# Optimization experiments

Measured on AMD Instinct MI355X. Metric: run time of the kernel, lower is better.

The kernel has to match this reference:

```python
import jax, jax.numpy as jnp
import numpy as np

D_IN, D_OUT, K = 128, 256, 16
B, N = 2, 16384
D_HALF = D_OUT // 2
EPS = 1e-6
GROUPS = 16


def conv1x1(x, w, b):
    # x: (B,C,N,K), w: (O,C), b: (O,)
    return jnp.einsum('oc,bcnk->bonk', w, x) + b[None, :, None, None]


def groupnorm(x, w, b, groups=GROUPS):
    Bv, C, Nv, Kv = x.shape
    xr = x.reshape(Bv, groups, C // groups, Nv, Kv)
    m = xr.mean(axis=(2, 3, 4), keepdims=True)
    v = xr.var(axis=(2, 3, 4), keepdims=True)
    xn = ((xr - m) / jnp.sqrt(v + EPS)).reshape(Bv, C, Nv, Kv)
    return xn * w[None, :, None, None] + b[None, :, None, None]


def lse(coords, x, idx, dist, w, b, gw, gb):
    # coords: (B,N,3); x: (B,C,N,1); idx: (B,N,K); dist: (B,N,K)
    nbr = jax.vmap(lambda c, i: c[i])(coords, idx)          # (B,N,K,3)
    ctr = jnp.broadcast_to(coords[:, :, None, :], nbr.shape)  # (B,N,K,3)
    rel = jnp.concatenate([ctr, nbr, ctr - nbr], axis=-1)    # (B,N,K,9)
    geo = jnp.concatenate([rel.transpose(0, 3, 1, 2), dist[:, None, :, :]], axis=1)  # (B,10,N,K)
    geo = jax.nn.relu(groupnorm(conv1x1(geo, w, b), gw, gb))  # (B,d/2,N,K)
    nf = jax.vmap(lambda f, i: f[:, i])(x[..., 0], idx)       # (B,d/2,N,K)
    return jnp.concatenate([geo, nf], axis=1)                 # (B,d,N,K)


def attentive_pool(x, w, b, gw, gb):
    m = x.mean(axis=-1, keepdims=True)  # (B,C,N,1)
    return jax.nn.relu(groupnorm(conv1x1(m, w, b), gw, gb))


def setup_inputs() -> dict:
    key = jax.random.key(0)
    ks = jax.random.split(key, 16)
    s = 0.02
    d = {
        'coords': jax.random.normal(ks[0], (B, N, 3), jnp.float32),
        'features': jax.random.normal(ks[1], (B, D_IN, N, 1), jnp.float32),
        'knn_dist': jax.random.uniform(ks[2], (B, N, K), jnp.float32),
        'knn_idx': jax.random.randint(ks[3], (B, N, K), 0, N),
        'w1': jax.random.normal(ks[4], (D_HALF, D_IN), jnp.float32) * s,
        'b1': jnp.zeros((D_HALF,), jnp.float32),
        'lse1_w': jax.random.normal(ks[5], (D_HALF, 10), jnp.float32) * s,
        'lse1_b': jnp.zeros((D_HALF,), jnp.float32),
        'lse1_gw': jnp.ones((D_HALF,), jnp.float32),
        'lse1_gb': jnp.zeros((D_HALF,), jnp.float32),
        'pool1_w': jax.random.normal(ks[6], (D_HALF, D_OUT), jnp.float32) * s,
        'pool1_b': jnp.zeros((D_HALF,), jnp.float32),
        'pool1_gw': jnp.ones((D_HALF,), jnp.float32),
        'pool1_gb': jnp.zeros((D_HALF,), jnp.float32),
        'lse2_w': jax.random.normal(ks[7], (D_HALF, 10), jnp.float32) * s,
        'lse2_b': jnp.zeros((D_HALF,), jnp.float32),
        'lse2_gw': jnp.ones((D_HALF,), jnp.float32),
        'lse2_gb': jnp.zeros((D_HALF,), jnp.float32),
        'pool2_w': jax.random.normal(ks[8], (D_OUT, D_OUT), jnp.float32) * s,
        'pool2_b': jnp.zeros((D_OUT,), jnp.float32),
        'pool2_gw': jnp.ones((D_OUT,), jnp.float32),
        'pool2_gb': jnp.zeros((D_OUT,), jnp.float32),
        'mlp2_w': jax.random.normal(ks[9], (2 * D_OUT, D_OUT), jnp.float32) * s,
        'mlp2_b': jnp.zeros((2 * D_OUT,), jnp.float32),
        'sc_w': jax.random.normal(ks[10], (2 * D_OUT, D_IN), jnp.float32) * s,
        'sc_b': jnp.zeros((2 * D_OUT,), jnp.float32),
        'sc_gw': jnp.ones((2 * D_OUT,), jnp.float32),
        'sc_gb': jnp.zeros((2 * D_OUT,), jnp.float32),
    }
    return d


def reference(coords, features, knn_dist, knn_idx,
              w1, b1,
              lse1_w, lse1_b, lse1_gw, lse1_gb,
              pool1_w, pool1_b, pool1_gw, pool1_gb,
              lse2_w, lse2_b, lse2_gw, lse2_gb,
              pool2_w, pool2_b, pool2_gw, pool2_gb,
              mlp2_w, mlp2_b, sc_w, sc_b, sc_gw, sc_gb):
    # mlp1: conv + LeakyReLU(0.2), no norm
    x = jax.nn.leaky_relu(conv1x1(features, w1, b1), 0.2)        # (B,d/2,N,1)
    x = lse(coords, x, knn_idx, knn_dist, lse1_w, lse1_b, lse1_gw, lse1_gb)  # (B,d,N,K)
    x = attentive_pool(x, pool1_w, pool1_b, pool1_gw, pool1_gb)  # (B,d/2,N,1)
    x = lse(coords, x, knn_idx, knn_dist, lse2_w, lse2_b, lse2_gw, lse2_gb)  # (B,d,N,K)
    x = attentive_pool(x, pool2_w, pool2_b, pool2_gw, pool2_gb)  # (B,d,N,1)
    main = conv1x1(x, mlp2_w, mlp2_b)                            # (B,2d,N,1)
    short = groupnorm(conv1x1(features, sc_w, sc_b), sc_gw, sc_gb)
    return jax.nn.leaky_relu(main + short, 0.01)                 # (B,2d,N,1)
```

## Files before the change

kernel.cpp:

```cpp
#include <hip/hip_runtime.h>


constexpr int Bc = 2;
constexpr int Nc = 16384;
constexpr int Kc = 16;
constexpr float EPSc = 1e-6f;

typedef __attribute__((ext_vector_type(8))) short short8;
typedef __attribute__((ext_vector_type(4))) short short4v;
typedef __attribute__((ext_vector_type(4))) float floatx4;

__device__ inline short f2bf(float x) {
    union { float f; unsigned u; } v; v.f = x;
    unsigned r = v.u + 0x7fffu + ((v.u >> 16) & 1u);
    return (short)(r >> 16);
}
__device__ inline float bf2f(short s) {
    union { unsigned u; float f; } v;
    v.u = ((unsigned)(unsigned short)s) << 16;
    return v.f;
}

constexpr size_t OW_P1W = 0;
constexpr size_t OW_P2W = OW_P1W + 128*256;
constexpr size_t OW_M2W = OW_P2W + 256*256;
constexpr size_t OW_SCW = OW_M2W + 512*256;
constexpr size_t OW_W1  = OW_SCW + 512*128;
constexpr size_t OW_L1W = OW_W1  + 128*128;
constexpr size_t OW_L2W = OW_L1W + 128*32;
constexpr size_t OW_FB  = OW_L2W + 128*32;
constexpr size_t OW_X1  = OW_FB  + (size_t)Bc*Nc*128;
constexpr size_t OW_M   = OW_X1  + (size_t)Bc*Nc*128;
constexpr size_t OW_Z1  = OW_M   + (size_t)Bc*Nc*256;
constexpr size_t OW_Z2  = OW_Z1  + (size_t)Bc*Nc*128;
constexpr size_t OW_S   = OW_Z2  + (size_t)Bc*Nc*256;

constexpr int CV0 = 128*256;
constexpr int CV1 = CV0 + 256*256;
constexpr int CV2 = CV1 + 512*256;
constexpr int CV3 = CV2 + 512*128;
constexpr int CV4 = CV3 + 128*128;
constexpr int CV5 = CV4 + 128*32;
constexpr int CV6 = CV5 + 128*32;
constexpr int CVTOT = CV6 + 512;

__global__ void prep_kernel(const float* __restrict__ p1w,
                            const float* __restrict__ p2w,
                            const float* __restrict__ m2w,
                            const float* __restrict__ scw,
                            const float* __restrict__ w1,
                            const float* __restrict__ l1w,
                            const float* __restrict__ l2w,
                            short* __restrict__ W16,
                            float* __restrict__ ST)
{
    int i = blockIdx.x * 256 + threadIdx.x;
    if (i < CV0) { W16[OW_P1W + i] = f2bf(p1w[i]); return; }
    if (i < CV1) { int k = i - CV0; W16[OW_P2W + k] = f2bf(p2w[k]); return; }
    if (i < CV2) { int k = i - CV1; W16[OW_M2W + k] = f2bf(m2w[k]); return; }
    if (i < CV3) { int k = i - CV2; W16[OW_SCW + k] = f2bf(scw[k]); return; }
    if (i < CV4) { int k = i - CV3; W16[OW_W1  + k] = f2bf(w1[k]); return; }
    if (i < CV5) { int k = i - CV4; int o = k >> 5, c = k & 31;
                   W16[OW_L1W + k] = (c < 10) ? f2bf(l1w[o*10+c]) : (short)0; return; }
    if (i < CV6) { int k = i - CV5; int o = k >> 5, c = k & 31;
                   W16[OW_L2W + k] = (c < 10) ? f2bf(l2w[o*10+c]) : (short)0; return; }
    { int k = i - CV6; if (k < 512) ST[k] = 0.f; }
}

__global__ void feat_t_kernel(const float* __restrict__ in, short* __restrict__ out) {
    int tid  = threadIdx.x;
    int lane = tid & 63, wave = tid >> 6;
    int bb = blockIdx.x / (Nc / 64);
    int n  = (blockIdx.x % (Nc / 64)) * 64 + lane;
    #pragma unroll
    for (int cc = 0; cc < 4; cc++) {
        int c0 = (wave + cc * 4) * 8;
        short8 sv;
        #pragma unroll
        for (int i = 0; i < 8; i++)
            sv[i] = f2bf(in[((size_t)bb * 128 + c0 + i) * Nc + n]);
        *(short8*)&out[((size_t)(bb * Nc + n)) * 128 + c0] = sv;
    }
}

__launch_bounds__(256)
__global__ void geo_reduce_kernel(const float* __restrict__ coords,
                                  const int* __restrict__ knn_idx,
                                  const float* __restrict__ knn_dist,
                                  float* __restrict__ dst)
{
    __shared__ float part[4][65];
    const int tid  = threadIdx.x;
    const int b    = blockIdx.y;
    const int base = blockIdx.x * 256 + tid;
    const float* cb  = coords   + (size_t)b * Nc * 3;
    const int*   ib  = knn_idx  + (size_t)b * Nc * Kc;
    const float* db  = knn_dist + (size_t)b * Nc * Kc;

    float acc[65];
    #pragma unroll
    for (int i = 0; i < 65; i++) acc[i] = 0.f;

    #pragma unroll
    for (int it = 0; it < 4; it++) {
        int r = base + it * 65536;
        int n = r >> 4;
        float cx = cb[n*3+0], cy = cb[n*3+1], cz = cb[n*3+2];
        int   j  = ib[r];
        float nx = cb[j*3+0], ny = cb[j*3+1], nz = cb[j*3+2];
        float d  = db[r];
        float g[10] = {cx,cy,cz,nx,ny,nz,cx-nx,cy-ny,cz-nz,d};
        #pragma unroll
        for (int c = 0; c < 10; c++) acc[c] += g[c];
        int idx = 10;
        #pragma unroll
        for (int c = 0; c < 10; c++)
            #pragma unroll
            for (int c2 = c; c2 < 10; c2++) acc[idx++] += g[c] * g[c2];
    }
    #pragma unroll
    for (int i = 0; i < 65; i++) {
        float v = acc[i];
        #pragma unroll
        for (int off = 1; off < 64; off <<= 1) v += __shfl_xor(v, off);
        acc[i] = v;
    }
    int lane = tid & 63, wave = tid >> 6;
    if (lane == 0) {
        #pragma unroll
        for (int i = 0; i < 65; i++) part[wave][i] = acc[i];
    }
    __syncthreads();
    if (tid < 65) {
        float s = part[0][tid] + part[1][tid] + part[2][tid] + part[3][tid];
        atomicAdd(&dst[b * 65 + tid], s);
    }
}

__launch_bounds__(512)
__global__ void lse_param_kernel(const float* __restrict__ geoS,
                                 const float* __restrict__ l1w,
                                 const float* __restrict__ l1b,
                                 const float* __restrict__ l1gw,
                                 const float* __restrict__ l1gb,
                                 const float* __restrict__ l2w,
                                 const float* __restrict__ l2b,
                                 const float* __restrict__ l2gw,
                                 const float* __restrict__ l2gb,
                                 float* __restrict__ lp)
{
    __shared__ float osum[512], osq[512];
    const int tid = threadIdx.x;
    const int s = tid >> 8, r = tid & 255, b = r >> 7, o = r & 127;
    const float* wf = s ? l2w : l1w;
    const float* bf = s ? l2b : l1b;
    const float* gwf = s ? l2gw : l1gw;
    const float* gbf = s ? l2gb : l1gb;
    const float NK = (float)(Nc * Kc);
    const float* S = geoS + b * 65;

    float w[10];
    #pragma unroll
    for (int c = 0; c < 10; c++) w[c] = wf[o * 10 + c];
    float wS = 0.f;
    #pragma unroll
    for (int c = 0; c < 10; c++) wS += w[c] * S[c];
    float q = 0.f;
    {
        int idx = 10;
        #pragma unroll
        for (int c = 0; c < 10; c++)
            #pragma unroll
            for (int c2 = c; c2 < 10; c2++) {
                float t = w[c] * w[c2] * S[idx++];
                q += (c == c2) ? t : 2.f * t;
            }
    }
    float bo = bf[o];
    osum[tid] = NK * bo + wS;
    osq[tid]  = NK * bo * bo + 2.f * bo * wS + q;
    __syncthreads();
    int gb0 = tid & ~7;
    float gs = 0.f, gq = 0.f;
    #pragma unroll
    for (int i = 0; i < 8; i++) { gs += osum[gb0 + i]; gq += osq[gb0 + i]; }
    float cnt  = 8.f * NK;
    float mean = gs / cnt;
    float var  = gq / cnt - mean * mean;
    float iv   = rsqrtf(var + EPSc);
    float psc  = iv * gwf[o];
    float psh  = (bo - mean) * psc + gbf[o];
    lp[s * 512 + b * 256 + o]       = psc;
    lp[s * 512 + b * 256 + 128 + o] = psh;
}

template<int CIN, int COUT, int GROUP_CH, int MODE>
__launch_bounds__(256)
__global__ void gemm_conv(const short* __restrict__ wA,
                          const short* __restrict__ xB,
                          const float* __restrict__ bias,
                          short* __restrict__ outb,
                          float* __restrict__ outf,
                          float* __restrict__ stats,
                          const short* __restrict__ sbuf,
                          const float* __restrict__ st_sc,
                          const float* __restrict__ gw,
                          const float* __restrict__ gb,
                          float sc_cnt,
                          const float* __restrict__ bst,
                          const float* __restrict__ bgw,
                          const float* __restrict__ bgb,
                          float bcnt,
                          const float* __restrict__ bias2,
                          short* __restrict__ outb2)
{
    __shared__ short Abuf[128 * 68];
    __shared__ short Bbuf[128 * 68];
    __shared__ float sstat[32];
    __shared__ float smean[4], sinv[4];
    __shared__ float bsc[256], bsh[256];

    const int tid  = threadIdx.x;
    const int n0   = blockIdx.x * 128;
    const int mo   = blockIdx.y * 128;
    const int b    = blockIdx.z;
    const int lane = tid & 63;
    const int wave = tid >> 6;
    const int wm   = (wave >> 1) * 64;
    const int wn   = (wave & 1) * 64;
    const int l15  = lane & 15;
    const int quad = lane >> 4;
    const bool sc_tile = (MODE == 4) && (mo < 512);

    if constexpr (MODE == 2 || MODE == 4) { if (tid < 32) sstat[tid] = 0.f; }
    if constexpr (MODE == 3) {
        if (tid < 4) {
            int g = (mo >> 5) + tid;
            float s0 = st_sc[(b * 16 + g) * 2 + 0];
            float s1 = st_sc[(b * 16 + g) * 2 + 1];
            float mean = s0 / sc_cnt;
            float var  = s1 / sc_cnt - mean * mean;
            smean[tid] = mean;
            sinv[tid]  = rsqrtf(var + EPSc);
        }
        if (tid < CIN) {
            int g = tid >> 4;
            float s0 = bst[(b * 16 + g) * 2 + 0];
            float s1 = bst[(b * 16 + g) * 2 + 1];
            float mean = s0 / bcnt;
            float var  = s1 / bcnt - mean * mean;
            float inv  = rsqrtf(var + EPSc);
            float sc_  = inv * bgw[tid];
            bsc[tid] = sc_;
            bsh[tid] = bgb[tid] - mean * sc_;
        }
    }

    floatx4 acc[4][4];
    #pragma unroll
    for (int mi = 0; mi < 4; mi++)
        #pragma unroll
        for (int ni = 0; ni < 4; ni++)
            acc[mi][ni] = (floatx4){0.f, 0.f, 0.f, 0.f};

    const short* wAr = wA + (size_t)mo * CIN;
    const short* xBr = xB + (size_t)b * Nc * CIN + (size_t)n0 * CIN;

    for (int c0 = 0; c0 < CIN; c0 += 64) {
        __syncthreads();
        #pragma unroll
        for (int s = 0; s < 4; s++) {
            int e = tid + s * 256;
            int r = e >> 3, q = e & 7;
            *(short8*)&Abuf[r * 68 + q * 8] =
                *(const short8*)(wAr + (size_t)r * CIN + c0 + q * 8);
            short8 v = *(const short8*)(xBr + (size_t)r * CIN + c0 + q * 8);
            if constexpr (MODE == 3) {
                #pragma unroll
                for (int i = 0; i < 8; i++) {
                    int ch = c0 + q * 8 + i;
                    float t = bf2f(v[i]) * bsc[ch] + bsh[ch];
                    v[i] = f2bf(t > 0.f ? t : 0.f);
                }
            }
            *(short8*)&Bbuf[r * 68 + q * 8] = v;
        }
        __syncthreads();

        #pragma unroll
        for (int kk = 0; kk < 2; kk++) {
            short8 af[4], bfr[4];
            #pragma unroll
            for (int mi = 0; mi < 4; mi++)
                af[mi] = *(short8*)&Abuf[(wm + mi * 16 + l15) * 68 + kk * 32 + quad * 8];
            #pragma unroll
            for (int ni = 0; ni < 4; ni++)
                bfr[ni] = *(short8*)&Bbuf[(wn + ni * 16 + l15) * 68 + kk * 32 + quad * 8];
            #pragma unroll
            for (int mi = 0; mi < 4; mi++)
                #pragma unroll
                for (int ni = 0; ni < 4; ni++)
                    acc[mi][ni] = __builtin_amdgcn_mfma_f32_16x16x32_bf16(
                        af[mi], bfr[ni], acc[mi][ni], 0, 0, 0);
        }
    }

    #pragma unroll
    for (int mi = 0; mi < 4; mi++) {
        int rowl = wm + mi * 16 + quad * 4;
        float b4[4], gw4[4], gb4[4];
        #pragma unroll
        for (int r = 0; r < 4; r++) {
            if constexpr (MODE == 4) {
                b4[r] = sc_tile ? bias[mo + rowl + r] : bias2[mo - 512 + rowl + r];
            } else {
                b4[r] = bias[mo + rowl + r];
            }
            if constexpr (MODE == 3) {
                gw4[r] = gw[mo + rowl + r];
                gb4[r] = gb[mo + rowl + r];
            }
        }
        float gs = 0.f, gq = 0.f;
        #pragma unroll
        for (int ni = 0; ni < 4; ni++) {
            int col = n0 + wn + ni * 16 + l15;
            if constexpr (MODE == 3) {
                short4v s4 = *(const short4v*)&sbuf[((size_t)(b * Nc + col)) * 512 + mo + rowl];
                int gl = rowl >> 5;
                #pragma unroll
                for (int r = 0; r < 4; r++) {
                    float v = acc[mi][ni][r] + b4[r];
                    float s = bf2f(s4[r]);
                    float sn = (s - smean[gl]) * sinv[gl] * gw4[r] + gb4[r];
                    float o = v + sn;
                    o = o > 0.f ? o : 0.01f * o;
                    outf[((size_t)b * COUT + mo + rowl + r) * Nc + col] = o;
                }
            } else if constexpr (MODE == 4) {
                short4v sv;
                #pragma unroll
                for (int r = 0; r < 4; r++) {
                    float v = acc[mi][ni][r] + b4[r];
                    if (sc_tile) { gs += v; gq += v * v; }
                    else v = v > 0.f ? v : 0.2f * v;
                    sv[r] = f2bf(v);
                }
                if (sc_tile)
                    *(short4v*)&outb[((size_t)(b * Nc + col)) * 512 + mo + rowl] = sv;
                else
                    *(short4v*)&outb2[((size_t)(b * Nc + col)) * 128 + mo - 512 + rowl] = sv;
            } else {
                short4v sv;
                #pragma unroll
                for (int r = 0; r < 4; r++) {
                    float v = acc[mi][ni][r] + b4[r];
                    if constexpr (MODE == 1) v = v > 0.f ? v : 0.2f * v;
                    if constexpr (MODE == 2) { gs += v; gq += v * v; }
                    sv[r] = f2bf(v);
                }
                *(short4v*)&outb[((size_t)(b * Nc + col)) * COUT + mo + rowl] = sv;
            }
        }
        if ((MODE == 2) || (MODE == 4 && sc_tile)) {
            #pragma unroll
            for (int off = 1; off < 16; off <<= 1) {
                gs += __shfl_xor(gs, off);
                gq += __shfl_xor(gq, off);
            }
            if (l15 == 0) {
                int gl = rowl / GROUP_CH;
                atomicAdd(&sstat[gl * 2 + 0], gs);
                atomicAdd(&sstat[gl * 2 + 1], gq);
            }
        }
    }
    if ((MODE == 2) || (MODE == 4 && sc_tile)) {
        __syncthreads();
        constexpr int NG = 128 / GROUP_CH;
        if (tid < 2 * NG) {
            int g0 = mo / GROUP_CH;
            atomicAdd(&stats[b * 32 + (g0 + (tid >> 1)) * 2 + (tid & 1)], sstat[tid]);
        }
    }
}

__launch_bounds__(256)
__global__ void lse_m_kernel(const float* __restrict__ coords,
                             const int* __restrict__ knn_idx,
                             const float* __restrict__ knn_dist,
                             const short* __restrict__ xprev,
                             const short* __restrict__ wpad,
                             const float* __restrict__ lp,
                             const float* __restrict__ xst,
                             const float* __restrict__ xgw,
                             const float* __restrict__ xgb,
                             float xcnt,
                             short* __restrict__ m)
{
    __shared__ short Bbuf[256 * 40];
    __shared__ int   jl[256];
    __shared__ float xscs[128], xshs[128];

    const int tid = threadIdx.x;
    const int b   = blockIdx.x >> 10;
    const int n0  = (blockIdx.x & 1023) * 16;
    const bool norm = (xst != nullptr);

    const int lane = tid & 63, wave = tid >> 6;
    const int l15 = lane & 15, quad = lane >> 4;

    short8 af0 = *(const short8*)(wpad + ((wave * 2 + 0) * 16 + l15) * 32 + quad * 8);
    short8 af1 = *(const short8*)(wpad + ((wave * 2 + 1) * 16 + l15) * 32 + quad * 8);
    floatx4 psc0 = *(const floatx4*)&lp[b * 256 + (wave * 2 + 0) * 16 + quad * 4];
    floatx4 psh0 = *(const floatx4*)&lp[b * 256 + 128 + (wave * 2 + 0) * 16 + quad * 4];
    floatx4 psc1 = *(const floatx4*)&lp[b * 256 + (wave * 2 + 1) * 16 + quad * 4];
    floatx4 psh1 = *(const floatx4*)&lp[b * 256 + 128 + (wave * 2 + 1) * 16 + quad * 4];

    if (norm && tid < 128) {
        int g = tid >> 3;
        float s0 = xst[(b * 16 + g) * 2 + 0];
        float s1 = xst[(b * 16 + g) * 2 + 1];
        float mean = s0 / xcnt;
        float var  = s1 / xcnt - mean * mean;
        float inv  = rsqrtf(var + EPSc);
        float sc_  = inv * xgw[tid];
        xscs[tid] = sc_;
        xshs[tid] = xgb[tid] - mean * sc_;
    }
    {
        int pt = tid & 15, k = tid >> 4;
        int n  = n0 + pt;
        const float* cb = coords + (size_t)b * Nc * 3;
        float cx = cb[n*3+0], cy = cb[n*3+1], cz = cb[n*3+2];
        int   j  = knn_idx[((size_t)b * Nc + n) * Kc + k];
        float nx = cb[j*3+0], ny = cb[j*3+1], nz = cb[j*3+2];
        float d  = knn_dist[((size_t)b * Nc + n) * Kc + k];
        int col = k * 16 + pt;
        short8 w0, w1, zz;
        w0[0]=f2bf(cx); w0[1]=f2bf(cy); w0[2]=f2bf(cz);
        w0[3]=f2bf(nx); w0[4]=f2bf(ny); w0[5]=f2bf(nz);
        w0[6]=f2bf(cx-nx); w0[7]=f2bf(cy-ny);
        w1[0]=f2bf(cz-nz); w1[1]=f2bf(d);
        #pragma unroll
        for (int i = 2; i < 8; i++) w1[i] = 0;
        #pragma unroll
        for (int i = 0; i < 8; i++) zz[i] = 0;
        *(short8*)&Bbuf[col * 40 + 0]  = w0;
        *(short8*)&Bbuf[col * 40 + 8]  = w1;
        *(short8*)&Bbuf[col * 40 + 16] = zz;
        *(short8*)&Bbuf[col * 40 + 24] = zz;
        jl[col] = j;
    }
    __syncthreads();

    #pragma unroll
    for (int mt2 = 0; mt2 < 2; mt2++) {
        const int mt = wave * 2 + mt2;
        const short8 af = mt2 ? af1 : af0;
        const floatx4 psc4 = mt2 ? psc1 : psc0;
        const floatx4 psh4 = mt2 ? psh1 : psh0;
        float s4[4] = {0.f, 0.f, 0.f, 0.f};
        #pragma unroll
        for (int nb = 0; nb < 8; nb++) {
            short8 f0 = *(short8*)&Bbuf[((nb * 2 + 0) * 16 + l15) * 40 + quad * 8];
            short8 f1 = *(short8*)&Bbuf[((nb * 2 + 1) * 16 + l15) * 40 + quad * 8];
            floatx4 a0 = __builtin_amdgcn_mfma_f32_16x16x32_bf16(
                af, f0, (floatx4){0.f, 0.f, 0.f, 0.f}, 0, 0, 0);
            floatx4 a1 = __builtin_amdgcn_mfma_f32_16x16x32_bf16(
                af, f1, (floatx4){0.f, 0.f, 0.f, 0.f}, 0, 0, 0);
            #pragma unroll
            for (int r = 0; r < 4; r++) {
                float v0 = a0[r] * psc4[r] + psh4[r];
                float v1 = a1[r] * psc4[r] + psh4[r];
                s4[r] += (v0 > 0.f ? v0 : 0.f) + (v1 > 0.f ? v1 : 0.f);
            }
        }
        short4v sv;
        #pragma unroll
        for (int r = 0; r < 4; r++) sv[r] = f2bf(s4[r] * (1.f / 16.f));
        *(short4v*)&m[((size_t)(b * Nc + n0 + l15)) * 256 + mt * 16 + quad * 4] = sv;
    }

    {
        const int tp = tid >> 4, cs = tid & 15;
        float sc8[8], sh8[8];
        if (norm) {
            #pragma unroll
            for (int i = 0; i < 8; i++) { sc8[i] = xscs[cs*8+i]; sh8[i] = xshs[cs*8+i]; }
        }
        float acc8[8];
        #pragma unroll
        for (int i = 0; i < 8; i++) acc8[i] = 0.f;
        #pragma unroll
        for (int k = 0; k < 16; k++) {
            int j = jl[k * 16 + tp];
            short8 v = *(const short8*)&xprev[((size_t)(b * Nc + j)) * 128 + cs * 8];
            if (norm) {
                #pragma unroll
                for (int i = 0; i < 8; i++) {
                    float t = bf2f(v[i]) * sc8[i] + sh8[i];
                    acc8[i] += t > 0.f ? t : 0.f;
                }
            } else {
                #pragma unroll
                for (int i = 0; i < 8; i++) acc8[i] += bf2f(v[i]);
            }
        }
        short8 sv;
        #pragma unroll
        for (int i = 0; i < 8; i++) sv[i] = f2bf(acc8[i] * (1.f / 16.f));
        *(short8*)&m[((size_t)(b * Nc + n0 + tp)) * 256 + 128 + cs * 8] = sv;
    }
}

extern "C" void kernel_launch(void* const* d_in, const int* in_sizes, int n_in,
                              void* d_out, int out_size, void* d_ws, size_t ws_size,
                              hipStream_t stream)
{
    const float* coords   = (const float*)d_in[0];
    const float* features = (const float*)d_in[1];
    const float* knn_dist = (const float*)d_in[2];
    const int*   knn_idx  = (const int*)  d_in[3];
    const float* w1       = (const float*)d_in[4];
    const float* b1       = (const float*)d_in[5];
    const float* lse1_w   = (const float*)d_in[6];
    const float* lse1_b   = (const float*)d_in[7];
    const float* lse1_gw  = (const float*)d_in[8];
    const float* lse1_gb  = (const float*)d_in[9];
    const float* pool1_w  = (const float*)d_in[10];
    const float* pool1_b  = (const float*)d_in[11];
    const float* pool1_gw = (const float*)d_in[12];
    const float* pool1_gb = (const float*)d_in[13];
    const float* lse2_w   = (const float*)d_in[14];
    const float* lse2_b   = (const float*)d_in[15];
    const float* lse2_gw  = (const float*)d_in[16];
    const float* lse2_gb  = (const float*)d_in[17];
    const float* pool2_w  = (const float*)d_in[18];
    const float* pool2_b  = (const float*)d_in[19];
    const float* pool2_gw = (const float*)d_in[20];
    const float* pool2_gb = (const float*)d_in[21];
    const float* mlp2_w   = (const float*)d_in[22];
    const float* mlp2_b   = (const float*)d_in[23];
    const float* sc_w     = (const float*)d_in[24];
    const float* sc_b     = (const float*)d_in[25];
    const float* sc_gw    = (const float*)d_in[26];
    const float* sc_gb    = (const float*)d_in[27];
    (void)in_sizes; (void)n_in; (void)out_size; (void)ws_size;

    float* ST = (float*)d_ws;
    float* ST_SC  = ST + 0;
    float* ST_P1  = ST + 64;
    float* ST_P2  = ST + 128;
    float* ST_GEO = ST + 256;
    float* ST_LP  = ST + 512;
    short* W16 = (short*)(ST + 2048);
    short* P1Wb = W16 + OW_P1W;
    short* P2Wb = W16 + OW_P2W;
    short* M2Wb = W16 + OW_M2W;
    short* SCWb = W16 + OW_SCW;
    short* L1Wb = W16 + OW_L1W;
    short* L2Wb = W16 + OW_L2W;
    short* FB   = W16 + OW_FB;
    short* X1B  = W16 + OW_X1;
    short* MB   = W16 + OW_M;
    short* Z1   = W16 + OW_Z1;
    short* Z2   = W16 + OW_Z2;
    short* SB   = W16 + OW_S;
    float* out  = (float*)d_out;

    prep_kernel<<<(CVTOT + 255) / 256, 256, 0, stream>>>(
        pool1_w, pool2_w, mlp2_w, sc_w, w1, lse1_w, lse2_w, W16, ST);
    feat_t_kernel<<<Bc * Nc / 64, 256, 0, stream>>>(features, FB);
    geo_reduce_kernel<<<dim3(256, Bc), 256, 0, stream>>>(
        coords, knn_idx, knn_dist, ST_GEO);
    lse_param_kernel<<<1, 512, 0, stream>>>(
        ST_GEO, lse1_w, lse1_b, lse1_gw, lse1_gb,
        lse2_w, lse2_b, lse2_gw, lse2_gb, ST_LP);

    gemm_conv<128,640,32,4><<<dim3(Nc/128, 5, Bc), 256, 0, stream>>>(
        SCWb, FB, sc_b, SB, nullptr, ST_SC, nullptr, nullptr, nullptr, nullptr, 0.f,
        nullptr, nullptr, nullptr, 0.f, b1, X1B);
    lse_m_kernel<<<Bc * Nc / 16, 256, 0, stream>>>(
        coords, knn_idx, knn_dist, X1B, L1Wb, ST_LP,
        nullptr, nullptr, nullptr, 0.f, MB);
    gemm_conv<256,128,8,2><<<dim3(Nc/128, 1, Bc), 256, 0, stream>>>(
        P1Wb, MB, pool1_b, Z1, nullptr, ST_P1, nullptr, nullptr, nullptr, nullptr, 0.f,
        nullptr, nullptr, nullptr, 0.f, nullptr, nullptr);
    lse_m_kernel<<<Bc * Nc / 16, 256, 0, stream>>>(
        coords, knn_idx, knn_dist, Z1, L2Wb, ST_LP + 512,
        ST_P1, pool1_gw, pool1_gb, (float)(8 * Nc), MB);
    gemm_conv<256,256,16,2><<<dim3(Nc/128, 2, Bc), 256, 0, stream>>>(
        P2Wb, MB, pool2_b, Z2, nullptr, ST_P2, nullptr, nullptr, nullptr, nullptr, 0.f,
        nullptr, nullptr, nullptr, 0.f, nullptr, nullptr);
    gemm_conv<256,512,32,3><<<dim3(Nc/128, 4, Bc), 256, 0, stream>>>(
        M2Wb, Z2, mlp2_b, nullptr, out, nullptr, SB, ST_SC, sc_gw, sc_gb,
        (float)(32 * Nc), ST_P2, pool2_gw, pool2_gb, (float)(16 * Nc),
        nullptr, nullptr);
}
```

Baseline: 305.6 us.

## Fuse LSE neighbor-mean kernel with attentive-pool GEMM via shared-memory tile

Merges the LSE kernel, which builds the pooled 256-channel vector per point, with the following pool 1x1-conv GEMM. Each 512-thread block now handles 64 points and keeps the pooled tile in swizzled LDS. It then runs the pool conv with MFMA, writes Z, and accumulates the groupnorm statistics. This removes the global write and re-read of the intermediate M buffer and two kernel launches. In exchange it uses more LDS per block, which may lower occupancy, and adds block-level syncs between the four geometry passes.

```diff
diff --git a/kernel.cpp b/kernel.cpp
--- a/kernel.cpp
+++ b/kernel.cpp
@@ -385,38 +385,37 @@
     }
 }
 
-__launch_bounds__(256)
-__global__ void lse_m_kernel(const float* __restrict__ coords,
-                             const int* __restrict__ knn_idx,
-                             const float* __restrict__ knn_dist,
-                             const short* __restrict__ xprev,
-                             const short* __restrict__ wpad,
-                             const float* __restrict__ lp,
-                             const float* __restrict__ xst,
-                             const float* __restrict__ xgw,
-                             const float* __restrict__ xgb,
-                             float xcnt,
-                             short* __restrict__ m)
+template<int PCOUT, int PGROUP>
+__launch_bounds__(512)
+__global__ void lse_pool_kernel(const float* __restrict__ coords,
+                                const int* __restrict__ knn_idx,
+                                const float* __restrict__ knn_dist,
+                                const short* __restrict__ xprev,
+                                const short* __restrict__ wpad,
+                                const float* __restrict__ lp,
+                                const float* __restrict__ xst,
+                                const float* __restrict__ xgw,
+                                const float* __restrict__ xgb,
+                                float xcnt,
+                                const short* __restrict__ pw,
+                                const float* __restrict__ pb,
+                                float* __restrict__ stats,
+                                short* __restrict__ z)
 {
     __shared__ short Bbuf[256 * 40];
-    __shared__ int   jl[256];
+    __shared__ short mld[64 * 256];
+    __shared__ int   jl[1024];
     __shared__ float xscs[128], xshs[128];
+    __shared__ float sstat[32];
 
     const int tid = threadIdx.x;
-    const int b   = blockIdx.x >> 10;
-    const int n0  = (blockIdx.x & 1023) * 16;
+    const int b   = blockIdx.x >> 8;
+    const int n0  = (blockIdx.x & 255) * 64;
     const bool norm = (xst != nullptr);
-
     const int lane = tid & 63, wave = tid >> 6;
     const int l15 = lane & 15, quad = lane >> 4;
 
-    short8 af0 = *(const short8*)(wpad + ((wave * 2 + 0) * 16 + l15) * 32 + quad * 8);
-    short8 af1 = *(const short8*)(wpad + ((wave * 2 + 1) * 16 + l15) * 32 + quad * 8);
-    floatx4 psc0 = *(const floatx4*)&lp[b * 256 + (wave * 2 + 0) * 16 + quad * 4];
-    floatx4 psh0 = *(const floatx4*)&lp[b * 256 + 128 + (wave * 2 + 0) * 16 + quad * 4];
-    floatx4 psc1 = *(const floatx4*)&lp[b * 256 + (wave * 2 + 1) * 16 + quad * 4];
-    floatx4 psh1 = *(const floatx4*)&lp[b * 256 + 128 + (wave * 2 + 1) * 16 + quad * 4];
-
+    if (tid < 32) sstat[tid] = 0.f;
     if (norm && tid < 128) {
         int g = tid >> 3;
         float s0 = xst[(b * 16 + g) * 2 + 0];
@@ -428,58 +427,65 @@
         xscs[tid] = sc_;
         xshs[tid] = xgb[tid] - mean * sc_;
     }
-    {
-        int pt = tid & 15, k = tid >> 4;
-        int n  = n0 + pt;
-        const float* cb = coords + (size_t)b * Nc * 3;
-        float cx = cb[n*3+0], cy = cb[n*3+1], cz = cb[n*3+2];
-        int   j  = knn_idx[((size_t)b * Nc + n) * Kc + k];
-        float nx = cb[j*3+0], ny = cb[j*3+1], nz = cb[j*3+2];
-        float d  = knn_dist[((size_t)b * Nc + n) * Kc + k];
-        int col = k * 16 + pt;
-        short8 w0, w1, zz;
-        w0[0]=f2bf(cx); w0[1]=f2bf(cy); w0[2]=f2bf(cz);
-        w0[3]=f2bf(nx); w0[4]=f2bf(ny); w0[5]=f2bf(nz);
-        w0[6]=f2bf(cx-nx); w0[7]=f2bf(cy-ny);
-        w1[0]=f2bf(cz-nz); w1[1]=f2bf(d);
-        #pragma unroll
-        for (int i = 2; i < 8; i++) w1[i] = 0;
-        #pragma unroll
-        for (int i = 0; i < 8; i++) zz[i] = 0;
-        *(short8*)&Bbuf[col * 40 + 0]  = w0;
-        *(short8*)&Bbuf[col * 40 + 8]  = w1;
-        *(short8*)&Bbuf[col * 40 + 16] = zz;
-        *(short8*)&Bbuf[col * 40 + 24] = zz;
-        jl[col] = j;
-    }
-    __syncthreads();
-
-    #pragma unroll
-    for (int mt2 = 0; mt2 < 2; mt2++) {
-        const int mt = wave * 2 + mt2;
-        const short8 af = mt2 ? af1 : af0;
-        const floatx4 psc4 = mt2 ? psc1 : psc0;
-        const floatx4 psh4 = mt2 ? psh1 : psh0;
-        float s4[4] = {0.f, 0.f, 0.f, 0.f};
-        #pragma unroll
-        for (int nb = 0; nb < 8; nb++) {
-            short8 f0 = *(short8*)&Bbuf[((nb * 2 + 0) * 16 + l15) * 40 + quad * 8];
-            short8 f1 = *(short8*)&Bbuf[((nb * 2 + 1) * 16 + l15) * 40 + quad * 8];
-            floatx4 a0 = __builtin_amdgcn_mfma_f32_16x16x32_bf16(
-                af, f0, (floatx4){0.f, 0.f, 0.f, 0.f}, 0, 0, 0);
-            floatx4 a1 = __builtin_amdgcn_mfma_f32_16x16x32_bf16(
-                af, f1, (floatx4){0.f, 0.f, 0.f, 0.f}, 0, 0, 0);
-            #pragma unroll
-            for (int r = 0; r < 4; r++) {
-                float v0 = a0[r] * psc4[r] + psh4[r];
-                float v1 = a1[r] * psc4[r] + psh4[r];
-                s4[r] += (v0 > 0.f ? v0 : 0.f) + (v1 > 0.f ? v1 : 0.f);
-            }
-        }
-        short4v sv;
-        #pragma unroll
-        for (int r = 0; r < 4; r++) sv[r] = f2bf(s4[r] * (1.f / 16.f));
-        *(short4v*)&m[((size_t)(b * Nc + n0 + l15)) * 256 + mt * 16 + quad * 4] = sv;
+
+    short8 af = *(const short8*)(wpad + (wave * 16 + l15) * 32 + quad * 8);
+    floatx4 psc = *(const floatx4*)&lp[b * 256 + wave * 16 + quad * 4];
+    floatx4 psh = *(const floatx4*)&lp[b * 256 + 128 + wave * 16 + quad * 4];
+
+    const float* cb = coords + (size_t)b * Nc * 3;
+
+    #pragma unroll
+    for (int pass = 0; pass < 4; pass++) {
+        if (tid < 256) {
+            int ptl = tid & 15, k = tid >> 4;
+            int p = pass * 16 + ptl;
+            int n = n0 + p;
+            float cx = cb[n*3+0], cy = cb[n*3+1], cz = cb[n*3+2];
+            int   j  = knn_idx[((size_t)b * Nc + n) * Kc + k];
+            float nx = cb[j*3+0], ny = cb[j*3+1], nz = cb[j*3+2];
+            float d  = knn_dist[((size_t)b * Nc + n) * Kc + k];
+            int col = k * 16 + ptl;
+            short8 w0, w1, zz;
+            w0[0]=f2bf(cx); w0[1]=f2bf(cy); w0[2]=f2bf(cz);
+            w0[3]=f2bf(nx); w0[4]=f2bf(ny); w0[5]=f2bf(nz);
+            w0[6]=f2bf(cx-nx); w0[7]=f2bf(cy-ny);
+            w1[0]=f2bf(cz-nz); w1[1]=f2bf(d);
+            #pragma unroll
+            for (int i = 2; i < 8; i++) w1[i] = 0;
+            #pragma unroll
+            for (int i = 0; i < 8; i++) zz[i] = 0;
+            *(short8*)&Bbuf[col * 40 + 0]  = w0;
+            *(short8*)&Bbuf[col * 40 + 8]  = w1;
+            *(short8*)&Bbuf[col * 40 + 16] = zz;
+            *(short8*)&Bbuf[col * 40 + 24] = zz;
+            jl[k * 64 + p] = j;
+        }
+        __syncthreads();
+        {
+            float s4[4] = {0.f, 0.f, 0.f, 0.f};
+            #pragma unroll
+            for (int nb = 0; nb < 8; nb++) {
+                short8 f0 = *(short8*)&Bbuf[((nb*2+0)*16 + l15) * 40 + quad * 8];
+                short8 f1 = *(short8*)&Bbuf[((nb*2+1)*16 + l15) * 40 + quad * 8];
+                floatx4 a0 = __builtin_amdgcn_mfma_f32_16x16x32_bf16(
+                    af, f0, (floatx4){0.f, 0.f, 0.f, 0.f}, 0, 0, 0);
+                floatx4 a1 = __builtin_amdgcn_mfma_f32_16x16x32_bf16(
+                    af, f1, (floatx4){0.f, 0.f, 0.f, 0.f}, 0, 0, 0);
+                #pragma unroll
+                for (int r = 0; r < 4; r++) {
+                    float v0 = a0[r] * psc[r] + psh[r];
+                    float v1 = a1[r] * psc[r] + psh[r];
+                    s4[r] += (v0 > 0.f ? v0 : 0.f) + (v1 > 0.f ? v1 : 0.f);
+                }
+            }
+            int p = pass * 16 + l15;
+            int g = wave * 2 + (quad >> 1);
+            short4v sv;
+            #pragma unroll
+            for (int r = 0; r < 4; r++) sv[r] = f2bf(s4[r] * (1.f / 16.f));
+            *(short4v*)&mld[p * 256 + ((g ^ (p & 7)) << 3) + (quad & 1) * 4] = sv;
+        }
+        __syncthreads();
     }
 
     {
@@ -489,29 +495,85 @@
             #pragma unroll
             for (int i = 0; i < 8; i++) { sc8[i] = xscs[cs*8+i]; sh8[i] = xshs[cs*8+i]; }
         }
-        float acc8[8];
-        #pragma unroll
-        for (int i = 0; i < 8; i++) acc8[i] = 0.f;
-        #pragma unroll
-        for (int k = 0; k < 16; k++) {
-            int j = jl[k * 16 + tp];
-            short8 v = *(const short8*)&xprev[((size_t)(b * Nc + j)) * 128 + cs * 8];
-            if (norm) {
-                #pragma unroll
-                for (int i = 0; i < 8; i++) {
-                    float t = bf2f(v[i]) * sc8[i] + sh8[i];
-                    acc8[i] += t > 0.f ? t : 0.f;
+        #pragma unroll
+        for (int pp = 0; pp < 2; pp++) {
+            int p = tp + pp * 32;
+            float acc8[8];
+            #pragma unroll
+            for (int i = 0; i < 8; i++) acc8[i] = 0.f;
+            #pragma unroll
+            for (int k = 0; k < 16; k++) {
+                int j = jl[k * 64 + p];
+                short8 v = *(const short8*)&xprev[((size_t)(b * Nc + j)) * 128 + cs * 8];
+                if (norm) {
+                    #pragma unroll
+                    for (int i = 0; i < 8; i++) {
+                        float t = bf2f(v[i]) * sc8[i] + sh8[i];
+                        acc8[i] += t > 0.f ? t : 0.f;
+                    }
+                } else {
+                    #pragma unroll
+                    for (int i = 0; i < 8; i++) acc8[i] += bf2f(v[i]);
                 }
-            } else {
-                #pragma unroll
-                for (int i = 0; i < 8; i++) acc8[i] += bf2f(v[i]);
-            }
-        }
-        short8 sv;
-        #pragma unroll
-        for (int i = 0; i < 8; i++) sv[i] = f2bf(acc8[i] * (1.f / 16.f));
-        *(short8*)&m[((size_t)(b * Nc + n0 + tp)) * 256 + 128 + cs * 8] = sv;
-    }
+            }
+            short8 sv;
+            #pragma unroll
+            for (int i = 0; i < 8; i++) sv[i] = f2bf(acc8[i] * (1.f / 16.f));
+            int g = 16 + cs;
+            *(short8*)&mld[p * 256 + ((g ^ (p & 7)) << 3)] = sv;
+        }
+    }
+    __syncthreads();
+
+    constexpr int NOT = PCOUT / 128;
+    #pragma unroll
+    for (int oi = 0; oi < NOT; oi++) {
+        const int ot = wave + oi * 8;
+        short8 afk[8];
+        #pragma unroll
+        for (int ks = 0; ks < 8; ks++)
+            afk[ks] = *(const short8*)(pw + ((size_t)(ot * 16 + l15)) * 256 + ks * 32 + quad * 8);
+        floatx4 acc[4];
+        #pragma unroll
+        for (int nt = 0; nt < 4; nt++) acc[nt] = (floatx4){0.f, 0.f, 0.f, 0.f};
+        #pragma unroll
+        for (int ks = 0; ks < 8; ks++) {
+            #pragma unroll
+            for (int nt = 0; nt < 4; nt++) {
+                int p = nt * 16 + l15;
+                int g = ks * 4 + quad;
+                short8 bfr = *(short8*)&mld[p * 256 + ((g ^ (p & 7)) << 3)];
+                acc[nt] = __builtin_amdgcn_mfma_f32_16x16x32_bf16(
+                    afk[ks], bfr, acc[nt], 0, 0, 0);
+            }
+        }
+        floatx4 b4 = *(const floatx4*)&pb[ot * 16 + quad * 4];
+        float gs = 0.f, gq = 0.f;
+        #pragma unroll
+        for (int nt = 0; nt < 4; nt++) {
+            int col = n0 + nt * 16 + l15;
+            short4v sv;
+            #pragma unroll
+            for (int r = 0; r < 4; r++) {
+                float v = acc[nt][r] + b4[r];
+                gs += v; gq += v * v;
+                sv[r] = f2bf(v);
+            }
+            *(short4v*)&z[((size_t)(b * Nc + col)) * PCOUT + ot * 16 + quad * 4] = sv;
+        }
+        #pragma unroll
+        for (int off = 1; off < 16; off <<= 1) {
+            gs += __shfl_xor(gs, off);
+            gq += __shfl_xor(gq, off);
+        }
+        if (l15 == 0) {
+            int gl = (ot * 16 + quad * 4) / PGROUP;
+            atomicAdd(&sstat[gl * 2 + 0], gs);
+            atomicAdd(&sstat[gl * 2 + 1], gq);
+        }
+    }
+    __syncthreads();
+    if (tid < 32) atomicAdd(&stats[b * 32 + tid], sstat[tid]);
 }
 
 extern "C" void kernel_launch(void* const* d_in, const int* in_sizes, int n_in,
@@ -563,7 +625,6 @@
     short* L2Wb = W16 + OW_L2W;
     short* FB   = W16 + OW_FB;
     short* X1B  = W16 + OW_X1;
-    short* MB   = W16 + OW_M;
     short* Z1   = W16 + OW_Z1;
     short* Z2   = W16 + OW_Z2;
     short* SB   = W16 + OW_S;
@@ -581,18 +642,14 @@
     gemm_conv<128,640,32,4><<<dim3(Nc/128, 5, Bc), 256, 0, stream>>>(
         SCWb, FB, sc_b, SB, nullptr, ST_SC, nullptr, nullptr, nullptr, nullptr, 0.f,
         nullptr, nullptr, nullptr, 0.f, b1, X1B);
-    lse_m_kernel<<<Bc * Nc / 16, 256, 0, stream>>>(
+    lse_pool_kernel<128,8><<<Bc * Nc / 64, 512, 0, stream>>>(
         coords, knn_idx, knn_dist, X1B, L1Wb, ST_LP,
-        nullptr, nullptr, nullptr, 0.f, MB);
-    gemm_conv<256,128,8,2><<<dim3(Nc/128, 1, Bc), 256, 0, stream>>>(
-        P1Wb, MB, pool1_b, Z1, nullptr, ST_P1, nullptr, nullptr, nullptr, nullptr, 0.f,
-        nullptr, nullptr, nullptr, 0.f, nullptr, nullptr);
-    lse_m_kernel<<<Bc * Nc / 16, 256, 0, stream>>>(
+        nullptr, nullptr, nullptr, 0.f,
+        P1Wb, pool1_b, ST_P1, Z1);
+    lse_pool_kernel<256,16><<<Bc * Nc / 64, 512, 0, stream>>>(
         coords, knn_idx, knn_dist, Z1, L2Wb, ST_LP + 512,
-        ST_P1, pool1_gw, pool1_gb, (float)(8 * Nc), MB);
-    gemm_conv<256,256,16,2><<<dim3(Nc/128, 2, Bc), 256, 0, stream>>>(
-        P2Wb, MB, pool2_b, Z2, nullptr, ST_P2, nullptr, nullptr, nullptr, nullptr, 0.f,
-        nullptr, nullptr, nullptr, 0.f, nullptr, nullptr);
+        ST_P1, pool1_gw, pool1_gb, (float)(8 * Nc),
+        P2Wb, pool2_b, ST_P2, Z2);
     gemm_conv<256,512,32,3><<<dim3(Nc/128, 4, Bc), 256, 0, stream>>>(
         M2Wb, Z2, mlp2_b, nullptr, out, nullptr, SB, ST_SC, sc_gw, sc_gb,
         (float)(32 * Nc), ST_P2, pool2_gw, pool2_gb, (float)(16 * Nc),
```

After: 289.1 us. 5.4% less time.
